# Performance work log

Hardware: AMD Instinct MI355X
Metric: run time of the kernel (lower is better)

Reference implementation:

```python
import jax, jax.numpy as jnp
import numpy as np

D_MODEL = 768
NUM_HEADS = 12
D_K = D_MODEL // NUM_HEADS
B, T = 2, 4096


def setup_inputs() -> dict:
    key = jax.random.key(0)
    ks = jax.random.split(key, 5)
    x = jax.random.normal(ks[0], (B, T, D_MODEL), dtype=jnp.float32)
    # causal mask: True = masked (matches masked_fill semantics)
    mask = jnp.triu(jnp.ones((T, T), dtype=bool), k=1)
    W_qkv = jax.random.normal(ks[1], (D_MODEL, 3 * D_MODEL), dtype=jnp.float32) / np.sqrt(D_MODEL)
    b_qkv = jax.random.normal(ks[2], (3 * D_MODEL,), dtype=jnp.float32) * 0.02
    W_out = jax.random.normal(ks[3], (D_MODEL, D_MODEL), dtype=jnp.float32) / np.sqrt(D_MODEL)
    b_out = jax.random.normal(ks[4], (D_MODEL,), dtype=jnp.float32) * 0.02
    return {"x": x, "mask": mask, "W_qkv": W_qkv, "b_qkv": b_qkv, "W_out": W_out, "b_out": b_out}


def reference(x, mask, W_qkv, b_qkv, W_out, b_out):
    Bb, Tt, C = x.shape
    qkv = x @ W_qkv + b_qkv                       # [B,T,3C]
    # torch: reshape(B,T,H,3*d_k).transpose(1,2) then chunk on last dim
    qkv = qkv.reshape(Bb, Tt, NUM_HEADS, 3, D_K)  # split each head's 3*d_k chunk
    qkv = jnp.transpose(qkv, (0, 2, 1, 3, 4))     # [B,H,T,3,d_k]
    q, k, v = qkv[..., 0, :], qkv[..., 1, :], qkv[..., 2, :]
    scores = jnp.einsum('bhqd,bhkd->bhqk', q, k) / np.sqrt(D_K)
    scores = jnp.where(mask[None, None], -jnp.inf, scores)
    attn = jax.nn.softmax(scores, axis=-1)
    context = jnp.einsum('bhqk,bhkd->bhqd', attn, v)
    context = jnp.transpose(context, (0, 2, 1, 3)).reshape(Bb, Tt, C)
    return context @ W_out + b_out
```

## Files before the change

### kernel.cpp

```cpp
#include <hip/hip_runtime.h>
#include <hip/hip_bf16.h>
#include <stdint.h>


typedef __attribute__((ext_vector_type(8))) short bf16x8;
typedef __attribute__((ext_vector_type(4))) short bf16x4;
typedef __attribute__((ext_vector_type(4))) float f32x4;

#define TT 4096
#define NH 12
#define DK 64
#define DMODEL 768
#define NQKV 2304

__device__ __forceinline__ unsigned short f2bf(float f) {
    union { float f; unsigned u; } v; v.f = f;
    unsigned u = v.u;
    return (unsigned short)((u + 0x7fffu + ((u >> 16) & 1u)) >> 16);
}
__device__ __forceinline__ unsigned fbits(float f) {
    union { float f; unsigned u; } v; v.f = f; return v.u;
}
__device__ __forceinline__ unsigned pack_bf2(float a, float b) {
    return __builtin_amdgcn_perm(fbits(b) + 0x8000u, fbits(a) + 0x8000u, 0x07060302u);
}
__device__ __forceinline__ void glds16(const void* g, void* l) {
    __builtin_amdgcn_global_load_lds(
        (const __attribute__((address_space(1))) void*)g,
        (__attribute__((address_space(3))) void*)l, 16, 0, 0);
}

__global__ __launch_bounds__(256)
void prep(const float* __restrict__ x, unsigned short* __restrict__ xb,
          const float* __restrict__ Wq, unsigned short* __restrict__ Wqt,
          const float* __restrict__ Wo, unsigned short* __restrict__ Wot) {
    int b = blockIdx.x;
    if (b < 6144) {
        int i = (b * 256 + threadIdx.x) * 4;
        float4 v = *(const float4*)(x + i);
        uint2 u;
        u.x = pack_bf2(v.x, v.y);
        u.y = pack_bf2(v.z, v.w);
        *(uint2*)(xb + i) = u;
        return;
    }
    __shared__ unsigned short tile[64][65];
    const float* W; unsigned short* Wt; int K, N, bx, by;
    if (b < 6144 + 432) {
        int bb = b - 6144; bx = bb % 36; by = bb / 36;
        W = Wq; Wt = Wqt; K = DMODEL; N = NQKV;
    } else {
        int bb = b - 6576; bx = bb % 12; by = bb / 12;
        W = Wo; Wt = Wot; K = DMODEL; N = DMODEL;
    }
    int k0 = by * 64, n0 = bx * 64;
    int c = threadIdx.x & 63;
    int r0 = threadIdx.x >> 6;
    for (int p = 0; p < 16; ++p) {
        int r = r0 + p * 4;
        tile[r][c] = f2bf(W[(size_t)(k0 + r) * N + n0 + c]);
    }
    __syncthreads();
    for (int p = 0; p < 16; ++p) {
        int n = r0 + p * 4;
        Wt[(size_t)(n0 + n) * K + k0 + c] = tile[c][n];
    }
}

__global__ __launch_bounds__(256, 3)
void gemm_qkv(const unsigned short* __restrict__ Amat, const unsigned short* __restrict__ Bmat,
              const float* __restrict__ bias, unsigned short* __restrict__ qb,
              unsigned short* __restrict__ kb, unsigned short* __restrict__ vtb) {
    __shared__ unsigned short As[128 * 64];
    __shared__ unsigned short Bs[128 * 64];
    const int K = DMODEL;
    int m0 = blockIdx.y * 128, n0 = blockIdx.x * 128;
    int tid = threadIdx.x, lane = tid & 63, w = tid >> 6;
    int wm = (w >> 1) * 64, wn = (w & 1) * 64;
    int quad = lane >> 4, lc = lane & 15;

    const unsigned short* agp[4]; const unsigned short* bgp[4];
    unsigned short* alp[4]; unsigned short* blp[4];
    for (int p = 0; p < 4; ++p) {
        int c = (w * 4 + p) * 64 + lane;
        int row = c >> 3, pc = c & 7;
        int gc = pc ^ (row & 7);
        agp[p] = Amat + (size_t)(m0 + row) * K + gc * 8;
        bgp[p] = Bmat + (size_t)(n0 + row) * K + gc * 8;
        alp[p] = &As[(w * 4 + p) * 512];
        blp[p] = &Bs[(w * 4 + p) * 512];
    }
    int foff[4][2];
    for (int mt = 0; mt < 4; ++mt)
        for (int h = 0; h < 2; ++h)
            foff[mt][h] = (mt * 16 + lc) * 64 + (((quad + 4 * h) ^ (lc & 7)) * 8);

    f32x4 acc[4][4];
    for (int a = 0; a < 4; ++a)
        for (int b2 = 0; b2 < 4; ++b2) acc[a][b2] = (f32x4){0.f, 0.f, 0.f, 0.f};

    for (int k0 = 0; k0 < K; k0 += 64) {
        for (int p = 0; p < 4; ++p) {
            glds16(agp[p] + k0, alp[p]);
            glds16(bgp[p] + k0, blp[p]);
        }
        __syncthreads();
        bf16x8 af[4][2], bfr[4][2];
        for (int mt = 0; mt < 4; ++mt)
            for (int h = 0; h < 2; ++h) {
                af[mt][h]  = *(const bf16x8*)(&As[wm * 64 + foff[mt][h]]);
                bfr[mt][h] = *(const bf16x8*)(&Bs[wn * 64 + foff[mt][h]]);
            }
        for (int mt = 0; mt < 4; ++mt)
            for (int nt = 0; nt < 4; ++nt) {
                acc[mt][nt] = __builtin_amdgcn_mfma_f32_16x16x32_bf16(
                    af[mt][0], bfr[nt][0], acc[mt][nt], 0, 0, 0);
                acc[mt][nt] = __builtin_amdgcn_mfma_f32_16x16x32_bf16(
                    af[mt][1], bfr[nt][1], acc[mt][nt], 0, 0, 0);
            }
        __syncthreads();
    }
    const float c2q = 0.18033688f;
    for (int mt = 0; mt < 4; ++mt) {
        int colv = m0 + wm + mt * 16 + quad * 4;
        float4 bv = *(const float4*)(bias + colv);
        int h = colv / 192;
        int r = colv - h * 192;
        int which = r >> 6;
        int d0 = r & 63;
        for (int nt = 0; nt < 4; ++nt) {
            int tok = n0 + wn + nt * 16 + lc;
            int b = tok >> 12, t = tok & 4095;
            size_t bh = (size_t)(b * NH + h);
            float v0 = acc[mt][nt][0] + bv.x, v1 = acc[mt][nt][1] + bv.y;
            float v2 = acc[mt][nt][2] + bv.z, v3 = acc[mt][nt][3] + bv.w;
            if (which == 0) {
                uint2 u;
                u.x = pack_bf2(v0 * c2q, v1 * c2q);
                u.y = pack_bf2(v2 * c2q, v3 * c2q);
                *(uint2*)(qb + (bh * TT + t) * DK + d0) = u;
            } else if (which == 1) {
                uint2 u;
                u.x = pack_bf2(v0, v1);
                u.y = pack_bf2(v2, v3);
                *(uint2*)(kb + (bh * TT + t) * DK + d0) = u;
            } else {
                unsigned short* vp = vtb + (bh * DK + d0) * TT + t;
                vp[0] = f2bf(v0); vp[TT] = f2bf(v1);
                vp[2 * TT] = f2bf(v2); vp[3 * TT] = f2bf(v3);
            }
        }
    }
}

template <bool DIAG>
__device__ __forceinline__ void flash_tile(const unsigned short* __restrict__ Kb,
                                           const unsigned short* __restrict__ Vb,
                                           bf16x8 qf0, bf16x8 qf1,
                                           f32x4 (&o)[4], f32x4& ol,
                                           int kt, int q_lo, int quad, int lc) {
    int c0 = quad ^ (lc & 7);
    int sw = lc & 7;
    const bf16x4 ones = {(short)0x3F80, (short)0x3F80, (short)0x3F80, (short)0x3F80};
    for (int ktile = 0; ktile < 4; ++ktile) {
        bf16x8 kf0 = *(const bf16x8*)(&Kb[(ktile * 16 + lc) * 64 + c0 * 8]);
        bf16x8 kf1 = *(const bf16x8*)(&Kb[(ktile * 16 + lc) * 64 + (c0 ^ 4) * 8]);
        f32x4 s = (f32x4){0.f, 0.f, 0.f, 0.f};
        s = __builtin_amdgcn_mfma_f32_16x16x32_bf16(kf0, qf0, s, 0, 0, 0);
        s = __builtin_amdgcn_mfma_f32_16x16x32_bf16(kf1, qf1, s, 0, 0, 0);
        float p[4];
        if (DIAG) {
            int key0 = kt + ktile * 16 + quad * 4;
            int qcol = q_lo + lc;
            for (int i = 0; i < 4; ++i) {
                float e = __builtin_amdgcn_exp2f(s[i]);
                if (key0 + i > qcol) e = 0.f;
                p[i] = e;
            }
        } else {
            for (int i = 0; i < 4; ++i) p[i] = __builtin_amdgcn_exp2f(s[i]);
        }
        union { uint2 u; bf16x4 v; } pc;
        pc.u.x = pack_bf2(p[0], p[1]);
        pc.u.y = pack_bf2(p[2], p[3]);
        ol = __builtin_amdgcn_mfma_f32_16x16x16bf16_1k(ones, pc.v, ol, 0, 0, 0);
        int c8 = (ktile * 2 + (quad >> 1)) ^ sw;
        int voff = c8 * 8 + (quad & 1) * 4;
        for (int dt = 0; dt < 4; ++dt) {
            bf16x4 vf = *(const bf16x4*)(&Vb[(dt * 16 + lc) * 64 + voff]);
            o[dt] = __builtin_amdgcn_mfma_f32_16x16x16bf16_1k(vf, pc.v, o[dt], 0, 0, 0);
        }
    }
}

__global__ __launch_bounds__(256)
void flash_attn(const unsigned short* __restrict__ qbuf,
                const unsigned short* __restrict__ kbuf,
                const unsigned short* __restrict__ vtbuf,
                unsigned short* __restrict__ ctx) {
    __shared__ unsigned short Ks[2][64 * 64];
    __shared__ unsigned short Vs[2][64 * 64];
    int bh = blockIdx.x;
    int qblk = 63 - (int)blockIdx.y;
    int tid = threadIdx.x, lane = tid & 63, w = tid >> 6;
    int quad = lane >> 4, lc = lane & 15;
    const size_t base = (size_t)bh * TT * DK;
    const unsigned short* kb = kbuf + base;
    const unsigned short* vb = vtbuf + base;
    int col8 = ((lane & 7) ^ (lane >> 3)) * 8;
    int klane = (lane >> 3) * DK + col8;
    int vlane = (lane >> 3) * TT + col8;
    size_t hb = (size_t)(bh / NH) * TT * DMODEL + (size_t)(bh % NH) * DK;

    int q_lo = qblk * 64 + w * 16;
    int ntile = qblk + 1;

    bf16x8 qf0, qf1;
    {
        const unsigned short* qp = qbuf + base + (size_t)(q_lo + lc) * DK;
        qf0 = *(const bf16x8*)(qp + quad * 8);
        qf1 = *(const bf16x8*)(qp + 32 + quad * 8);
    }
    f32x4 o[4];
    for (int dt = 0; dt < 4; ++dt) o[dt] = (f32x4){0.f, 0.f, 0.f, 0.f};
    f32x4 ol = (f32x4){0.f, 0.f, 0.f, 0.f};

    {
        int rb = (w & 1) * 4;
        if (w < 2)
            for (int r = 0; r < 4; ++r)
                glds16(kb + (size_t)((rb + r) * 8) * DK + klane, &Ks[0][(rb + r) * 512]);
        else
            for (int r = 0; r < 4; ++r)
                glds16(vb + (size_t)((rb + r) * 8) * TT + vlane, &Vs[0][(rb + r) * 512]);
    }
    __syncthreads();

    for (int ti = 0; ti < ntile; ++ti) {
        int cur = ti & 1;
        if (ti + 1 < ntile) {
            int kn = (ti + 1) * 64;
            int rb = (w & 1) * 4;
            if (w < 2)
                for (int r = 0; r < 4; ++r)
                    glds16(kb + (size_t)(kn + (rb + r) * 8) * DK + klane,
                           &Ks[cur ^ 1][(rb + r) * 512]);
            else
                for (int r = 0; r < 4; ++r)
                    glds16(vb + (size_t)((rb + r) * 8) * TT + kn + vlane,
                           &Vs[cur ^ 1][(rb + r) * 512]);
        }
        int kt = ti * 64;
        if (ti == ntile - 1)
            flash_tile<true>(&Ks[cur][0], &Vs[cur][0], qf0, qf1, o, ol,
                             kt, q_lo, quad, lc);
        else
            flash_tile<false>(&Ks[cur][0], &Vs[cur][0], qf0, qf1, o, ol,
                              kt, q_lo, quad, lc);
        __syncthreads();
    }

    float inv = 1.f / ol[0];
    int t = q_lo + lc;
    unsigned short* cp = ctx + hb + (size_t)t * DMODEL;
    for (int dt = 0; dt < 4; ++dt) {
        uint2 u;
        u.x = pack_bf2(o[dt][0] * inv, o[dt][1] * inv);
        u.y = pack_bf2(o[dt][2] * inv, o[dt][3] * inv);
        *(uint2*)(cp + dt * 16 + quad * 4) = u;
    }
}

__global__ __launch_bounds__(256, 4)
void gemm_out(const unsigned short* __restrict__ Amat, const unsigned short* __restrict__ Bmat,
              const float* __restrict__ bias, float* __restrict__ out) {
    __shared__ unsigned short S[(64 + 128) * 64];
    const int K = DMODEL;
    int m0 = blockIdx.y * 64, n0 = blockIdx.x * 128;
    int tid = threadIdx.x, lane = tid & 63, w = tid >> 6;
    int wm = (w & 1) * 32, wn = (w >> 1) * 64;
    int quad = lane >> 4, lc = lane & 15;

    const unsigned short* gp[6]; unsigned short* lp[6];
    for (int p = 0; p < 6; ++p) {
        int c = (w * 6 + p) * 64 + lane;
        if (c < 512) {
            int row = c >> 3, gc = (c & 7) ^ (row & 7);
            gp[p] = Amat + (size_t)(m0 + row) * K + gc * 8;
        } else {
            int cb = c - 512;
            int row = cb >> 3, gc = (cb & 7) ^ (row & 7);
            gp[p] = Bmat + (size_t)(n0 + row) * K + gc * 8;
        }
        lp[p] = &S[(w * 6 + p) * 512];
    }
    int foffA[2][2], foffB[4][2];
    for (int mt = 0; mt < 2; ++mt)
        for (int h = 0; h < 2; ++h)
            foffA[mt][h] = (wm + mt * 16 + lc) * 64 + (((quad + 4 * h) ^ (lc & 7)) * 8);
    for (int nt = 0; nt < 4; ++nt)
        for (int h = 0; h < 2; ++h)
            foffB[nt][h] = 4096 + (wn + nt * 16 + lc) * 64 + (((quad + 4 * h) ^ (lc & 7)) * 8);

    f32x4 acc[2][4];
    for (int a = 0; a < 2; ++a)
        for (int b2 = 0; b2 < 4; ++b2) acc[a][b2] = (f32x4){0.f, 0.f, 0.f, 0.f};

    for (int k0 = 0; k0 < K; k0 += 64) {
        for (int p = 0; p < 6; ++p) glds16(gp[p] + k0, lp[p]);
        __syncthreads();
        bf16x8 af[2][2], bfr[4][2];
        for (int mt = 0; mt < 2; ++mt)
            for (int h = 0; h < 2; ++h) af[mt][h] = *(const bf16x8*)(&S[foffA[mt][h]]);
        for (int nt = 0; nt < 4; ++nt)
            for (int h = 0; h < 2; ++h) bfr[nt][h] = *(const bf16x8*)(&S[foffB[nt][h]]);
        for (int mt = 0; mt < 2; ++mt)
            for (int nt = 0; nt < 4; ++nt) {
                acc[mt][nt] = __builtin_amdgcn_mfma_f32_16x16x32_bf16(
                    af[mt][0], bfr[nt][0], acc[mt][nt], 0, 0, 0);
                acc[mt][nt] = __builtin_amdgcn_mfma_f32_16x16x32_bf16(
                    af[mt][1], bfr[nt][1], acc[mt][nt], 0, 0, 0);
            }
        __syncthreads();
    }
    for (int mt = 0; mt < 2; ++mt) {
        int colv = m0 + wm + mt * 16 + quad * 4;
        float4 bv = *(const float4*)(bias + colv);
        for (int nt = 0; nt < 4; ++nt) {
            int tok = n0 + wn + nt * 16 + lc;
            float4 ov;
            ov.x = acc[mt][nt][0] + bv.x;
            ov.y = acc[mt][nt][1] + bv.y;
            ov.z = acc[mt][nt][2] + bv.z;
            ov.w = acc[mt][nt][3] + bv.w;
            *(float4*)(out + (size_t)tok * DMODEL + colv) = ov;
        }
    }
}

extern "C" void kernel_launch(void* const* d_in, const int* in_sizes, int n_in,
                              void* d_out, int out_size, void* d_ws, size_t ws_size,
                              hipStream_t stream) {
    const float* x     = (const float*)d_in[0];
    const float* W_qkv = (const float*)d_in[2];
    const float* b_qkv = (const float*)d_in[3];
    const float* W_out = (const float*)d_in[4];
    const float* b_out = (const float*)d_in[5];
    float* out = (float*)d_out;

    unsigned short* ws = (unsigned short*)d_ws;
    unsigned short* Wqkv_t = ws;
    unsigned short* Wout_t = Wqkv_t + (size_t)NQKV * DMODEL;
    unsigned short* q_buf  = Wout_t + (size_t)DMODEL * DMODEL;
    unsigned short* k_buf  = q_buf  + (size_t)2 * NH * TT * DK;
    unsigned short* vt_buf = k_buf  + (size_t)2 * NH * TT * DK;
    unsigned short* ctx    = vt_buf + (size_t)2 * NH * TT * DK;
    unsigned short* x_bf   = ctx;

    prep<<<dim3(6720), 256, 0, stream>>>(x, x_bf, W_qkv, Wqkv_t, W_out, Wout_t);
    gemm_qkv<<<dim3((2 * TT) / 128, NQKV / 128), 256, 0, stream>>>(
        Wqkv_t, x_bf, b_qkv, q_buf, k_buf, vt_buf);
    flash_attn<<<dim3(2 * NH, TT / 64), 256, 0, stream>>>(q_buf, k_buf, vt_buf, ctx);
    gemm_out<<<dim3((2 * TT) / 128, DMODEL / 64), 256, 0, stream>>>(
        Wout_t, ctx, b_out, out);
}
```

Before: 260.0 us.

## Process two 16-row query groups per wave to reuse K/V fragments

Each wave in the flash attention kernel now handles 32 query rows (two 16-row groups) instead of 16, so the block shrinks from 256 to 128 threads for the same 64-query tile. K and V fragments loaded from LDS are reused across both query groups, halving LDS reads per MFMA. The two remaining waves each load a full K or V tile (8 glds16 each). This raises register pressure (doubled accumulators) and halves the waves per block, which may reduce latency hiding.

```diff
diff --git a/kernel.cpp b/kernel.cpp
--- a/kernel.cpp
+++ b/kernel.cpp
@@ -156,8 +156,8 @@
 template <bool DIAG>
 __device__ __forceinline__ void flash_tile(const unsigned short* __restrict__ Kb,
                                            const unsigned short* __restrict__ Vb,
-                                           bf16x8 qf0, bf16x8 qf1,
-                                           f32x4 (&o)[4], f32x4& ol,
+                                           const bf16x8 (&qf)[2][2],
+                                           f32x4 (&o)[2][4], f32x4 (&ol)[2],
                                            int kt, int q_lo, int quad, int lc) {
     int c0 = quad ^ (lc & 7);
     int sw = lc & 7;
@@ -165,35 +165,38 @@
     for (int ktile = 0; ktile < 4; ++ktile) {
         bf16x8 kf0 = *(const bf16x8*)(&Kb[(ktile * 16 + lc) * 64 + c0 * 8]);
         bf16x8 kf1 = *(const bf16x8*)(&Kb[(ktile * 16 + lc) * 64 + (c0 ^ 4) * 8]);
-        f32x4 s = (f32x4){0.f, 0.f, 0.f, 0.f};
-        s = __builtin_amdgcn_mfma_f32_16x16x32_bf16(kf0, qf0, s, 0, 0, 0);
-        s = __builtin_amdgcn_mfma_f32_16x16x32_bf16(kf1, qf1, s, 0, 0, 0);
-        float p[4];
-        if (DIAG) {
-            int key0 = kt + ktile * 16 + quad * 4;
-            int qcol = q_lo + lc;
-            for (int i = 0; i < 4; ++i) {
-                float e = __builtin_amdgcn_exp2f(s[i]);
-                if (key0 + i > qcol) e = 0.f;
-                p[i] = e;
-            }
-        } else {
-            for (int i = 0; i < 4; ++i) p[i] = __builtin_amdgcn_exp2f(s[i]);
-        }
-        union { uint2 u; bf16x4 v; } pc;
-        pc.u.x = pack_bf2(p[0], p[1]);
-        pc.u.y = pack_bf2(p[2], p[3]);
-        ol = __builtin_amdgcn_mfma_f32_16x16x16bf16_1k(ones, pc.v, ol, 0, 0, 0);
+        union { uint2 u; bf16x4 v; } pc[2];
+        for (int qg = 0; qg < 2; ++qg) {
+            f32x4 s = (f32x4){0.f, 0.f, 0.f, 0.f};
+            s = __builtin_amdgcn_mfma_f32_16x16x32_bf16(kf0, qf[qg][0], s, 0, 0, 0);
+            s = __builtin_amdgcn_mfma_f32_16x16x32_bf16(kf1, qf[qg][1], s, 0, 0, 0);
+            float p[4];
+            if (DIAG) {
+                int key0 = kt + ktile * 16 + quad * 4;
+                int qcol = q_lo + qg * 16 + lc;
+                for (int i = 0; i < 4; ++i) {
+                    float e = __builtin_amdgcn_exp2f(s[i]);
+                    if (key0 + i > qcol) e = 0.f;
+                    p[i] = e;
+                }
+            } else {
+                for (int i = 0; i < 4; ++i) p[i] = __builtin_amdgcn_exp2f(s[i]);
+            }
+            pc[qg].u.x = pack_bf2(p[0], p[1]);
+            pc[qg].u.y = pack_bf2(p[2], p[3]);
+            ol[qg] = __builtin_amdgcn_mfma_f32_16x16x16bf16_1k(ones, pc[qg].v, ol[qg], 0, 0, 0);
+        }
         int c8 = (ktile * 2 + (quad >> 1)) ^ sw;
         int voff = c8 * 8 + (quad & 1) * 4;
         for (int dt = 0; dt < 4; ++dt) {
             bf16x4 vf = *(const bf16x4*)(&Vb[(dt * 16 + lc) * 64 + voff]);
-            o[dt] = __builtin_amdgcn_mfma_f32_16x16x16bf16_1k(vf, pc.v, o[dt], 0, 0, 0);
-        }
-    }
-}
-
-__global__ __launch_bounds__(256)
+            o[0][dt] = __builtin_amdgcn_mfma_f32_16x16x16bf16_1k(vf, pc[0].v, o[0][dt], 0, 0, 0);
+            o[1][dt] = __builtin_amdgcn_mfma_f32_16x16x16bf16_1k(vf, pc[1].v, o[1][dt], 0, 0, 0);
+        }
+    }
+}
+
+__global__ __launch_bounds__(128)
 void flash_attn(const unsigned short* __restrict__ qbuf,
                 const unsigned short* __restrict__ kbuf,
                 const unsigned short* __restrict__ vtbuf,
@@ -212,27 +215,29 @@
     int vlane = (lane >> 3) * TT + col8;
     size_t hb = (size_t)(bh / NH) * TT * DMODEL + (size_t)(bh % NH) * DK;
 
-    int q_lo = qblk * 64 + w * 16;
+    int q_lo = qblk * 64 + w * 32;
     int ntile = qblk + 1;
 
-    bf16x8 qf0, qf1;
+    bf16x8 qf[2][2];
+    for (int qg = 0; qg < 2; ++qg) {
+        const unsigned short* qp = qbuf + base + (size_t)(q_lo + qg * 16 + lc) * DK;
+        qf[qg][0] = *(const bf16x8*)(qp + quad * 8);
+        qf[qg][1] = *(const bf16x8*)(qp + 32 + quad * 8);
+    }
+    f32x4 o[2][4];
+    for (int qg = 0; qg < 2; ++qg)
+        for (int dt = 0; dt < 4; ++dt) o[qg][dt] = (f32x4){0.f, 0.f, 0.f, 0.f};
+    f32x4 ol[2];
+    ol[0] = (f32x4){0.f, 0.f, 0.f, 0.f};
+    ol[1] = (f32x4){0.f, 0.f, 0.f, 0.f};
+
     {
-        const unsigned short* qp = qbuf + base + (size_t)(q_lo + lc) * DK;
-        qf0 = *(const bf16x8*)(qp + quad * 8);
-        qf1 = *(const bf16x8*)(qp + 32 + quad * 8);
-    }
-    f32x4 o[4];
-    for (int dt = 0; dt < 4; ++dt) o[dt] = (f32x4){0.f, 0.f, 0.f, 0.f};
-    f32x4 ol = (f32x4){0.f, 0.f, 0.f, 0.f};
-
-    {
-        int rb = (w & 1) * 4;
-        if (w < 2)
-            for (int r = 0; r < 4; ++r)
-                glds16(kb + (size_t)((rb + r) * 8) * DK + klane, &Ks[0][(rb + r) * 512]);
+        if (w == 0)
+            for (int r = 0; r < 8; ++r)
+                glds16(kb + (size_t)(r * 8) * DK + klane, &Ks[0][r * 512]);
         else
-            for (int r = 0; r < 4; ++r)
-                glds16(vb + (size_t)((rb + r) * 8) * TT + vlane, &Vs[0][(rb + r) * 512]);
+            for (int r = 0; r < 8; ++r)
+                glds16(vb + (size_t)(r * 8) * TT + vlane, &Vs[0][r * 512]);
     }
     __syncthreads();
 
@@ -240,34 +245,35 @@
         int cur = ti & 1;
         if (ti + 1 < ntile) {
             int kn = (ti + 1) * 64;
-            int rb = (w & 1) * 4;
-            if (w < 2)
-                for (int r = 0; r < 4; ++r)
-                    glds16(kb + (size_t)(kn + (rb + r) * 8) * DK + klane,
-                           &Ks[cur ^ 1][(rb + r) * 512]);
+            if (w == 0)
+                for (int r = 0; r < 8; ++r)
+                    glds16(kb + (size_t)(kn + r * 8) * DK + klane,
+                           &Ks[cur ^ 1][r * 512]);
             else
-                for (int r = 0; r < 4; ++r)
-                    glds16(vb + (size_t)((rb + r) * 8) * TT + kn + vlane,
-                           &Vs[cur ^ 1][(rb + r) * 512]);
+                for (int r = 0; r < 8; ++r)
+                    glds16(vb + (size_t)(r * 8) * TT + kn + vlane,
+                           &Vs[cur ^ 1][r * 512]);
         }
         int kt = ti * 64;
         if (ti == ntile - 1)
-            flash_tile<true>(&Ks[cur][0], &Vs[cur][0], qf0, qf1, o, ol,
+            flash_tile<true>(&Ks[cur][0], &Vs[cur][0], qf, o, ol,
                              kt, q_lo, quad, lc);
         else
-            flash_tile<false>(&Ks[cur][0], &Vs[cur][0], qf0, qf1, o, ol,
+            flash_tile<false>(&Ks[cur][0], &Vs[cur][0], qf, o, ol,
                               kt, q_lo, quad, lc);
         __syncthreads();
     }
 
-    float inv = 1.f / ol[0];
-    int t = q_lo + lc;
-    unsigned short* cp = ctx + hb + (size_t)t * DMODEL;
-    for (int dt = 0; dt < 4; ++dt) {
-        uint2 u;
-        u.x = pack_bf2(o[dt][0] * inv, o[dt][1] * inv);
-        u.y = pack_bf2(o[dt][2] * inv, o[dt][3] * inv);
-        *(uint2*)(cp + dt * 16 + quad * 4) = u;
+    for (int qg = 0; qg < 2; ++qg) {
+        float inv = 1.f / ol[qg][0];
+        int t = q_lo + qg * 16 + lc;
+        unsigned short* cp = ctx + hb + (size_t)t * DMODEL;
+        for (int dt = 0; dt < 4; ++dt) {
+            uint2 u;
+            u.x = pack_bf2(o[qg][dt][0] * inv, o[qg][dt][1] * inv);
+            u.y = pack_bf2(o[qg][dt][2] * inv, o[qg][dt][3] * inv);
+            *(uint2*)(cp + dt * 16 + quad * 4) = u;
+        }
     }
 }
 
@@ -360,7 +366,7 @@
     prep<<<dim3(6720), 256, 0, stream>>>(x, x_bf, W_qkv, Wqkv_t, W_out, Wout_t);
     gemm_qkv<<<dim3((2 * TT) / 128, NQKV / 128), 256, 0, stream>>>(
         Wqkv_t, x_bf, b_qkv, q_buf, k_buf, vt_buf);
-    flash_attn<<<dim3(2 * NH, TT / 64), 256, 0, stream>>>(q_buf, k_buf, vt_buf, ctx);
+    flash_attn<<<dim3(2 * NH, TT / 64), 128, 0, stream>>>(q_buf, k_buf, vt_buf, ctx);
     gemm_out<<<dim3((2 * TT) / 128, DMODEL / 64), 256, 0, stream>>>(
         Wout_t, ctx, b_out, out);
 }
```

Measured after the change: 284.0 us. 1.09x slower.
